# Kernel optimization log

Hardware: AMD Instinct MI355X
Metric: run time of the kernel (lower is better)

The kernel has to match this reference:

```python
import jax, jax.numpy as jnp
import numpy as np

B, S, D, H = 2, 2048, 1024, 16
DK = D // H


def setup_inputs() -> dict:
    key = jax.random.key(0)
    ks = jax.random.split(key, 12)
    scale = 1.0 / np.sqrt(D)
    inp = {
        "Q": jax.random.normal(ks[0], (B, S, D), jnp.float32),
        "K": jax.random.normal(ks[1], (B, S, D), jnp.float32),
        "V": jax.random.normal(ks[2], (B, S, D), jnp.float32),
        # causal mask, broadcast over batch: [B, S, S]
        "mask": jnp.broadcast_to(jnp.tril(jnp.ones((S, S), jnp.bool_)), (B, S, S)),
        "WQ_w": jax.random.normal(ks[3], (D, D), jnp.float32) * scale,
        "WQ_b": jnp.zeros((D,), jnp.float32),
        "WK_w": jax.random.normal(ks[4], (D, D), jnp.float32) * scale,
        "WK_b": jnp.zeros((D,), jnp.float32),
        "WV_w": jax.random.normal(ks[5], (D, D), jnp.float32) * scale,
        "WV_b": jnp.zeros((D,), jnp.float32),
        "WO_w": jax.random.normal(ks[6], (D, D), jnp.float32) * scale,
        "WO_b": jnp.zeros((D,), jnp.float32),
    }
    return inp


def reference(Q, K, V, mask, WQ_w, WQ_b, WK_w, WK_b, WV_w, WV_b, WO_w, WO_b):
    # Linear projections (torch Linear: x @ W.T + b), split heads -> [B,H,S,DK]
    def proj(x, w, b):
        return (x @ w.T + b).reshape(B, S, H, DK).transpose(0, 2, 1, 3)

    q = proj(Q, WQ_w, WQ_b)
    k = proj(K, WK_w, WK_b)
    v = proj(V, WV_w, WV_b)

    scores = jnp.einsum("bhqd,bhkd->bhqk", q, k) / jnp.sqrt(jnp.asarray(DK, q.dtype))
    scores = jnp.where(mask[:, None, :, :], scores, -jnp.inf)
    attn = jax.nn.softmax(scores, axis=-1)  # dropout is identity in eval mode

    out = jnp.einsum("bhqk,bhkd->bhqd", attn, v)
    out = out.transpose(0, 2, 1, 3).reshape(B, S, D)
    out = out @ WO_w.T + WO_b
    return (out, attn)
```

## Files before the change

kernel.cpp:

```cpp
#include <hip/hip_runtime.h>

#define S_LEN 2048
#define DMODEL 1024
#define NHEAD 16
#define DKH 64
#define BATCH 2

typedef __bf16 bf16_t;
typedef __bf16 bf16x8 __attribute__((ext_vector_type(8)));
typedef __bf16 bf16x4 __attribute__((ext_vector_type(4)));
typedef float f32x4 __attribute__((ext_vector_type(4)));

__device__ __forceinline__ void gload16(const bf16_t* g, bf16_t* l) {
  __builtin_amdgcn_global_load_lds(
      (const __attribute__((address_space(1))) unsigned int*)g,
      (__attribute__((address_space(3))) unsigned int*)l,
      16, 0, 0);
}

__global__ void cvt_all(const float* __restrict__ Q, const float* __restrict__ K,
                        const float* __restrict__ V, const float* __restrict__ WQ,
                        const float* __restrict__ WK, const float* __restrict__ WV,
                        const float* __restrict__ WO, bf16_t* __restrict__ dst) {
  const int i = blockIdx.x * 256 + threadIdx.x;
  const float* src;
  int off;
  if (i < 1572864) {
    const int seg = i >> 19;
    off = i & 524287;
    src = (seg == 0) ? Q : ((seg == 1) ? K : V);
  } else {
    const int j = i - 1572864;
    const int seg = j >> 17;
    off = j & 131071;
    src = (seg == 0) ? WQ : ((seg == 1) ? WK : ((seg == 2) ? WV : WO));
  }
  f32x4 a = *(const f32x4*)(src + (size_t)off * 8);
  f32x4 b = *(const f32x4*)(src + (size_t)off * 8 + 4);
  bf16x8 v;
#pragma unroll
  for (int j = 0; j < 4; ++j) { v[j] = (bf16_t)a[j]; v[4 + j] = (bf16_t)b[j]; }
  *(bf16x8*)(dst + (size_t)i * 8) = v;
}

struct GOp {
  const bf16_t* A;
  const bf16_t* W;
  const float* bias;
  char* out;
  int emode;
};

#define GM 4096
#define GN 1024
#define GK 1024
#define BM 128
#define BN 128
#define BK 64

__launch_bounds__(256, 2)
__global__ void gemm_bf16(GOp op0, GOp op1, GOp op2) {
  GOp op = (blockIdx.z == 0) ? op0 : ((blockIdx.z == 1) ? op1 : op2);
  const int n0 = blockIdx.x * BN;
  const int m0 = blockIdx.y * BM;
  const int t = threadIdx.x;
  const int w = t >> 6;
  const int l = t & 63;
  const int wr = w >> 1, wc = w & 1;
  const int lg = l >> 4, ll = l & 15;

  __shared__ __align__(16) bf16_t Asm[BM * BK];
  __shared__ __align__(16) bf16_t Bsm[BN * BK];

  f32x4 acc[4][4] = {};

  const int sr = l >> 3;
  const int sc = l & 7;

  for (int kt = 0; kt < GK / BK; ++kt) {
    __syncthreads();
#pragma unroll
    for (int i = 0; i < 4; ++i) {
      const int rbase = i * 32 + (w << 3);
      const int row = rbase + sr;
      const int gc = (sc ^ (row & 7)) << 3;
      gload16(op.A + (size_t)(m0 + row) * GK + kt * BK + gc, &Asm[rbase * BK]);
      gload16(op.W + (size_t)(n0 + row) * GK + kt * BK + gc, &Bsm[rbase * BK]);
    }
    __syncthreads();

    bf16x8 af[4][2], bfr[4][2];
#pragma unroll
    for (int mi = 0; mi < 4; ++mi) {
      const int row = wr * 64 + mi * 16 + ll;
      af[mi][0] = *(const bf16x8*)&Asm[row * BK + ((lg ^ (row & 7)) << 3)];
      af[mi][1] = *(const bf16x8*)&Asm[row * BK + (((4 + lg) ^ (row & 7)) << 3)];
    }
#pragma unroll
    for (int ni = 0; ni < 4; ++ni) {
      const int row = wc * 64 + ni * 16 + ll;
      bfr[ni][0] = *(const bf16x8*)&Bsm[row * BK + ((lg ^ (row & 7)) << 3)];
      bfr[ni][1] = *(const bf16x8*)&Bsm[row * BK + (((4 + lg) ^ (row & 7)) << 3)];
    }
#pragma unroll
    for (int mi = 0; mi < 4; ++mi)
#pragma unroll
      for (int ni = 0; ni < 4; ++ni) {
        acc[mi][ni] = __builtin_amdgcn_mfma_f32_16x16x32_bf16(af[mi][0], bfr[ni][0], acc[mi][ni], 0, 0, 0);
        acc[mi][ni] = __builtin_amdgcn_mfma_f32_16x16x32_bf16(af[mi][1], bfr[ni][1], acc[mi][ni], 0, 0, 0);
      }
  }

#pragma unroll
  for (int mi = 0; mi < 4; ++mi) {
#pragma unroll
    for (int ni = 0; ni < 4; ++ni) {
      const int col = n0 + wc * 64 + ni * 16 + ll;
      const int rbase = m0 + wr * 64 + mi * 16 + (lg << 2);
      const float bval = op.bias[col];
      f32x4 v = acc[mi][ni];
      if (op.emode == 0) {
        bf16_t* o = (bf16_t*)op.out;
#pragma unroll
        for (int r = 0; r < 4; ++r)
          o[(size_t)(rbase + r) * GN + col] = (bf16_t)(v[r] + bval);
      } else if (op.emode == 1) {
        const int hh = col >> 6, dd = col & 63;
        const int bb = rbase >> 11, ss = rbase & (S_LEN - 1);
        bf16_t* o = (bf16_t*)op.out + (((size_t)bb * NHEAD + hh) * DKH + dd) * S_LEN + ss;
        bf16x4 pk;
#pragma unroll
        for (int r = 0; r < 4; ++r) pk[r] = (bf16_t)(v[r] + bval);
        *(bf16x4*)o = pk;
      } else {
        float* o = (float*)op.out;
#pragma unroll
        for (int r = 0; r < 4; ++r)
          o[(size_t)(rbase + r) * GN + col] = v[r] + bval;
      }
    }
  }
}

__launch_bounds__(256, 2)
__global__ void attn2(const bf16_t* __restrict__ qp, const bf16_t* __restrict__ kp,
                      const bf16_t* __restrict__ vT, float* __restrict__ attn_out,
                      bf16_t* __restrict__ ctx) {
  const int raw = blockIdx.x;
  const int wg = (raw & 7) * 64 + (raw >> 3);
  const int bh = wg >> 4;
  const int pr = wg & 15;
  const int b = bh >> 4, h = bh & 15;
  const int flip = wg & 1;

  __shared__ __align__(16) bf16_t Qs[64 * 64];
  __shared__ __align__(16) bf16_t Ks[64 * 64];
  __shared__ __align__(16) bf16_t Vs[64 * 64];
  __shared__ __align__(16) bf16_t Pt[4][16 * 64];

  const int t = threadIdx.x;
  const int w = t >> 6;
  const int l = t & 63;
  const int lg = l >> 4;
  const int ll = l & 15;
  const int sr = l >> 3;
  const int sc = l & 7;

  for (int half = 0; half < 2; ++half) {
    const int qt = (half ^ flip) ? (31 - pr) : pr;
    const int q0 = qt * 64;
    const int nkt = qt + 1;

    __syncthreads();
#pragma unroll
    for (int i = 0; i < 2; ++i) {
      const int rbase = i * 32 + (w << 3);
      const int row = rbase + sr;
      const int gc = (sc ^ (row & 7)) << 3;
      gload16(qp + (size_t)(b * S_LEN + q0 + row) * DMODEL + h * DKH + gc, &Qs[rbase * 64]);
    }
    __syncthreads();

    bf16x8 qf0, qf1;
    {
      const int row = w * 16 + ll;
      qf0 = *(const bf16x8*)&Qs[row * 64 + ((lg ^ (row & 7)) << 3)];
      qf1 = *(const bf16x8*)&Qs[row * 64 + (((4 + lg) ^ (row & 7)) << 3)];
    }

    f32x4 oacc[4] = {};
    float sums[4] = {0.f, 0.f, 0.f, 0.f};
    const int qrow_base = q0 + w * 16 + (lg << 2);

    for (int kt = 0; kt < nkt; ++kt) {
      __syncthreads();
#pragma unroll
      for (int i = 0; i < 2; ++i) {
        const int rbase = i * 32 + (w << 3);
        const int row = rbase + sr;
        const int gc = (sc ^ (row & 7)) << 3;
        gload16(kp + (size_t)(b * S_LEN + kt * 64 + row) * DMODEL + h * DKH + gc, &Ks[rbase * 64]);
        gload16(vT + ((size_t)bh * DKH + row) * S_LEN + kt * 64 + gc, &Vs[rbase * 64]);
      }
      __syncthreads();

      const bool diag = (kt == qt);
#pragma unroll
      for (int cb = 0; cb < 4; ++cb) {
        const int krow = cb * 16 + ll;
        bf16x8 kf0 = *(const bf16x8*)&Ks[krow * 64 + ((lg ^ (krow & 7)) << 3)];
        bf16x8 kf1 = *(const bf16x8*)&Ks[krow * 64 + (((4 + lg) ^ (krow & 7)) << 3)];
        f32x4 a = {0.f, 0.f, 0.f, 0.f};
        a = __builtin_amdgcn_mfma_f32_16x16x32_bf16(qf0, kf0, a, 0, 0, 0);
        a = __builtin_amdgcn_mfma_f32_16x16x32_bf16(qf1, kf1, a, 0, 0, 0);
        const int gcol = kt * 64 + krow;
        if (diag) {
#pragma unroll
          for (int r = 0; r < 4; ++r) {
            const float e = (gcol <= qrow_base + r) ? __expf(a[r] * 0.125f) : 0.0f;
            sums[r] += e;
            const int ql = (lg << 2) + r;
            const int k = cb * 16 + ll;
            *(bf16_t*)((char*)&Pt[w][0] + ql * 128 + (((k >> 3) ^ (ql & 7)) << 4) + ((k & 7) << 1)) = (bf16_t)e;
          }
        } else {
#pragma unroll
          for (int r = 0; r < 4; ++r) {
            const float e = __expf(a[r] * 0.125f);
            sums[r] += e;
            const int ql = (lg << 2) + r;
            const int k = cb * 16 + ll;
            *(bf16_t*)((char*)&Pt[w][0] + ql * 128 + (((k >> 3) ^ (ql & 7)) << 4) + ((k & 7) << 1)) = (bf16_t)e;
          }
        }
      }
      bf16x8 pa0 = *(const bf16x8*)((char*)&Pt[w][0] + ll * 128 + ((lg ^ (ll & 7)) << 4));
      bf16x8 pa1 = *(const bf16x8*)((char*)&Pt[w][0] + ll * 128 + (((4 + lg) ^ (ll & 7)) << 4));
#pragma unroll
      for (int db = 0; db < 4; ++db) {
        const int drow = db * 16 + ll;
        bf16x8 vf0 = *(const bf16x8*)&Vs[drow * 64 + ((lg ^ (drow & 7)) << 3)];
        bf16x8 vf1 = *(const bf16x8*)&Vs[drow * 64 + (((4 + lg) ^ (drow & 7)) << 3)];
        oacc[db] = __builtin_amdgcn_mfma_f32_16x16x32_bf16(pa0, vf0, oacc[db], 0, 0, 0);
        oacc[db] = __builtin_amdgcn_mfma_f32_16x16x32_bf16(pa1, vf1, oacc[db], 0, 0, 0);
      }
    }

    float rinv[4];
#pragma unroll
    for (int r = 0; r < 4; ++r) {
      float s = sums[r];
      s += __shfl_xor(s, 1);
      s += __shfl_xor(s, 2);
      s += __shfl_xor(s, 4);
      s += __shfl_xor(s, 8);
      rinv[r] = 1.0f / s;
    }

#pragma unroll
    for (int db = 0; db < 4; ++db)
#pragma unroll
      for (int r = 0; r < 4; ++r) {
        const int grow = q0 + w * 16 + (lg << 2) + r;
        ctx[(size_t)(b * S_LEN + grow) * DMODEL + h * DKH + db * 16 + ll] = (bf16_t)(oacc[db][r] * rinv[r]);
      }

    float* arow = attn_out + ((size_t)bh * S_LEN + q0) * S_LEN;
    for (int kt = 0; kt <= qt; ++kt) {
      __syncthreads();
#pragma unroll
      for (int i = 0; i < 2; ++i) {
        const int rbase = i * 32 + (w << 3);
        const int row = rbase + sr;
        const int gc = (sc ^ (row & 7)) << 3;
        gload16(kp + (size_t)(b * S_LEN + kt * 64 + row) * DMODEL + h * DKH + gc, &Ks[rbase * 64]);
      }
      __syncthreads();

      const bool diag = (kt == qt);
#pragma unroll
      for (int cb = 0; cb < 4; ++cb) {
        const int krow = cb * 16 + ll;
        bf16x8 kf0 = *(const bf16x8*)&Ks[krow * 64 + ((lg ^ (krow & 7)) << 3)];
        bf16x8 kf1 = *(const bf16x8*)&Ks[krow * 64 + (((4 + lg) ^ (krow & 7)) << 3)];
        f32x4 a = {0.f, 0.f, 0.f, 0.f};
        a = __builtin_amdgcn_mfma_f32_16x16x32_bf16(qf0, kf0, a, 0, 0, 0);
        a = __builtin_amdgcn_mfma_f32_16x16x32_bf16(qf1, kf1, a, 0, 0, 0);
        const int gcol = kt * 64 + krow;
        if (diag) {
#pragma unroll
          for (int r = 0; r < 4; ++r) {
            const float e = (gcol <= qrow_base + r) ? __expf(a[r] * 0.125f) * rinv[r] : 0.0f;
            arow[(size_t)(w * 16 + (lg << 2) + r) * S_LEN + gcol] = e;
          }
        } else {
#pragma unroll
          for (int r = 0; r < 4; ++r)
            arow[(size_t)(w * 16 + (lg << 2) + r) * S_LEN + gcol] = __expf(a[r] * 0.125f) * rinv[r];
        }
      }
    }
    for (int kt = qt + 1; kt < 32; ++kt) {
      f32x4 z = {0.f, 0.f, 0.f, 0.f};
#pragma unroll
      for (int j = 0; j < 4; ++j) {
        const int row = w * 16 + (lg << 2) + j;
        *(f32x4*)(arow + (size_t)row * S_LEN + kt * 64 + (ll << 2)) = z;
      }
    }
  }
}

extern "C" void kernel_launch(void* const* d_in, const int* in_sizes, int n_in,
                              void* d_out, int out_size, void* d_ws, size_t ws_size,
                              hipStream_t stream) {
  const float* Q   = (const float*)d_in[0];
  const float* K   = (const float*)d_in[1];
  const float* V   = (const float*)d_in[2];
  const float* WQw = (const float*)d_in[4];
  const float* WQb = (const float*)d_in[5];
  const float* WKw = (const float*)d_in[6];
  const float* WKb = (const float*)d_in[7];
  const float* WVw = (const float*)d_in[8];
  const float* WVb = (const float*)d_in[9];
  const float* WOw = (const float*)d_in[10];
  const float* WOb = (const float*)d_in[11];

  char* ws = (char*)d_ws;
  bf16_t* qb  = (bf16_t*)(ws);
  bf16_t* kb  = (bf16_t*)(ws + (size_t)( 8 << 20));
  bf16_t* vb  = (bf16_t*)(ws + (size_t)(16 << 20));
  bf16_t* wq  = (bf16_t*)(ws + (size_t)(24 << 20));
  bf16_t* wk  = (bf16_t*)(ws + (size_t)(26 << 20));
  bf16_t* wv  = (bf16_t*)(ws + (size_t)(28 << 20));
  bf16_t* wo  = (bf16_t*)(ws + (size_t)(30 << 20));
  bf16_t* qp  = (bf16_t*)(ws + (size_t)(32 << 20));
  bf16_t* kp  = (bf16_t*)(ws + (size_t)(40 << 20));
  bf16_t* vT  = (bf16_t*)(ws + (size_t)(48 << 20));
  bf16_t* ctx = (bf16_t*)(ws + (size_t)(56 << 20));

  float* out_main = (float*)d_out;
  float* attn_out = out_main + (size_t)BATCH * S_LEN * DMODEL;

  cvt_all<<<dim3(8192), 256, 0, stream>>>(Q, K, V, WQw, WKw, WVw, WOw, (bf16_t*)ws);

  GOp opq{qb, wq, WQb, (char*)qp, 0};
  GOp opk{kb, wk, WKb, (char*)kp, 0};
  GOp opv{vb, wv, WVb, (char*)vT, 1};
  gemm_bf16<<<dim3(8, 32, 3), 256, 0, stream>>>(opq, opk, opv);

  attn2<<<dim3(512), 256, 0, stream>>>(qp, kp, vT, attn_out, ctx);

  GOp opo{ctx, wo, WOb, (char*)out_main, 2};
  gemm_bf16<<<dim3(8, 32, 1), 256, 0, stream>>>(opo, opo, opo);
}
```

Before: 224.5 us.

## Double-buffer LDS tiles in GEMM and attention kernels to overlap loads

Both the projection GEMM and the attention kernel now use two LDS buffers per operand. The next K/V (or A/W) tile is prefetched with global_load_lds while the current tile feeds the MFMAs, which replaces the load-then-sync pattern at the top of each iteration with a single barrier at the end. The aim is to hide global-memory latency behind matrix compute. The cost is doubled LDS use: 64KB per GEMM block, which could limit occupancy. The attention kernel is probably still bound by the large fp32 attention-matrix writes.

```diff
diff --git a/kernel.cpp b/kernel.cpp
--- a/kernel.cpp
+++ b/kernel.cpp
@@ -57,6 +57,7 @@
 #define BM 128
 #define BN 128
 #define BK 64
+#define NKT_G (GK / BK)
 
 __launch_bounds__(256, 2)
 __global__ void gemm_bf16(GOp op0, GOp op1, GOp op2) {
@@ -68,39 +69,46 @@
   const int l = t & 63;
   const int wr = w >> 1, wc = w & 1;
   const int lg = l >> 4, ll = l & 15;
-
-  __shared__ __align__(16) bf16_t Asm[BM * BK];
-  __shared__ __align__(16) bf16_t Bsm[BN * BK];
-
-  f32x4 acc[4][4] = {};
-
   const int sr = l >> 3;
   const int sc = l & 7;
 
-  for (int kt = 0; kt < GK / BK; ++kt) {
-    __syncthreads();
-#pragma unroll
-    for (int i = 0; i < 4; ++i) {
-      const int rbase = i * 32 + (w << 3);
-      const int row = rbase + sr;
-      const int gc = (sc ^ (row & 7)) << 3;
-      gload16(op.A + (size_t)(m0 + row) * GK + kt * BK + gc, &Asm[rbase * BK]);
-      gload16(op.W + (size_t)(n0 + row) * GK + kt * BK + gc, &Bsm[rbase * BK]);
-    }
-    __syncthreads();
+  __shared__ __align__(16) bf16_t Asm[2][BM * BK];
+  __shared__ __align__(16) bf16_t Bsm[2][BM * BK];
+
+  f32x4 acc[4][4] = {};
+
+  const bf16_t* Abase = op.A + (size_t)m0 * GK;
+  const bf16_t* Wbase = op.W + (size_t)n0 * GK;
+
+#define G_STAGE(bu, kt)                                                          \
+  {                                                                              \
+    _Pragma("unroll") for (int i = 0; i < 4; ++i) {                              \
+      const int rbase = i * 32 + (w << 3);                                       \
+      const int row = rbase + sr;                                                \
+      const int gc = (sc ^ (row & 7)) << 3;                                      \
+      gload16(Abase + (size_t)row * GK + (kt) * BK + gc, &Asm[bu][rbase * BK]);  \
+      gload16(Wbase + (size_t)row * GK + (kt) * BK + gc, &Bsm[bu][rbase * BK]);  \
+    }                                                                            \
+  }
+
+  G_STAGE(0, 0);
+  __syncthreads();
+  int cur = 0;
+  for (int kt = 0; kt < NKT_G; ++kt) {
+    if (kt + 1 < NKT_G) G_STAGE(cur ^ 1, kt + 1);
 
     bf16x8 af[4][2], bfr[4][2];
 #pragma unroll
     for (int mi = 0; mi < 4; ++mi) {
       const int row = wr * 64 + mi * 16 + ll;
-      af[mi][0] = *(const bf16x8*)&Asm[row * BK + ((lg ^ (row & 7)) << 3)];
-      af[mi][1] = *(const bf16x8*)&Asm[row * BK + (((4 + lg) ^ (row & 7)) << 3)];
+      af[mi][0] = *(const bf16x8*)&Asm[cur][row * BK + ((lg ^ (row & 7)) << 3)];
+      af[mi][1] = *(const bf16x8*)&Asm[cur][row * BK + (((4 + lg) ^ (row & 7)) << 3)];
     }
 #pragma unroll
     for (int ni = 0; ni < 4; ++ni) {
       const int row = wc * 64 + ni * 16 + ll;
-      bfr[ni][0] = *(const bf16x8*)&Bsm[row * BK + ((lg ^ (row & 7)) << 3)];
-      bfr[ni][1] = *(const bf16x8*)&Bsm[row * BK + (((4 + lg) ^ (row & 7)) << 3)];
+      bfr[ni][0] = *(const bf16x8*)&Bsm[cur][row * BK + ((lg ^ (row & 7)) << 3)];
+      bfr[ni][1] = *(const bf16x8*)&Bsm[cur][row * BK + (((4 + lg) ^ (row & 7)) << 3)];
     }
 #pragma unroll
     for (int mi = 0; mi < 4; ++mi)
@@ -109,6 +117,8 @@
         acc[mi][ni] = __builtin_amdgcn_mfma_f32_16x16x32_bf16(af[mi][0], bfr[ni][0], acc[mi][ni], 0, 0, 0);
         acc[mi][ni] = __builtin_amdgcn_mfma_f32_16x16x32_bf16(af[mi][1], bfr[ni][1], acc[mi][ni], 0, 0, 0);
       }
+    __syncthreads();
+    cur ^= 1;
   }
 
 #pragma unroll
@@ -154,8 +164,8 @@
   const int flip = wg & 1;
 
   __shared__ __align__(16) bf16_t Qs[64 * 64];
-  __shared__ __align__(16) bf16_t Ks[64 * 64];
-  __shared__ __align__(16) bf16_t Vs[64 * 64];
+  __shared__ __align__(16) bf16_t Ks[2][64 * 64];
+  __shared__ __align__(16) bf16_t Vs[2][64 * 64];
   __shared__ __align__(16) bf16_t Pt[4][16 * 64];
 
   const int t = threadIdx.x;
@@ -166,6 +176,30 @@
   const int sr = l >> 3;
   const int sc = l & 7;
 
+  const bf16_t* kbh = kp + (size_t)b * S_LEN * DMODEL + h * DKH;
+  const bf16_t* vbh = vT + (size_t)bh * DKH * S_LEN;
+
+#define KV_STAGE(bu, kt)                                                        \
+  {                                                                             \
+    _Pragma("unroll") for (int i = 0; i < 2; ++i) {                             \
+      const int rbase = i * 32 + (w << 3);                                      \
+      const int row = rbase + sr;                                               \
+      const int gc = (sc ^ (row & 7)) << 3;                                     \
+      gload16(kbh + (size_t)((kt) * 64 + row) * DMODEL + gc, &Ks[bu][rbase * 64]); \
+      gload16(vbh + (size_t)row * S_LEN + (kt) * 64 + gc, &Vs[bu][rbase * 64]); \
+    }                                                                           \
+  }
+
+#define K_STAGE(bu, kt)                                                         \
+  {                                                                             \
+    _Pragma("unroll") for (int i = 0; i < 2; ++i) {                             \
+      const int rbase = i * 32 + (w << 3);                                      \
+      const int row = rbase + sr;                                               \
+      const int gc = (sc ^ (row & 7)) << 3;                                     \
+      gload16(kbh + (size_t)((kt) * 64 + row) * DMODEL + gc, &Ks[bu][rbase * 64]); \
+    }                                                                           \
+  }
+
   for (int half = 0; half < 2; ++half) {
     const int qt = (half ^ flip) ? (31 - pr) : pr;
     const int q0 = qt * 64;
@@ -179,6 +213,7 @@
       const int gc = (sc ^ (row & 7)) << 3;
       gload16(qp + (size_t)(b * S_LEN + q0 + row) * DMODEL + h * DKH + gc, &Qs[rbase * 64]);
     }
+    KV_STAGE(0, 0);
     __syncthreads();
 
     bf16x8 qf0, qf1;
@@ -192,24 +227,16 @@
     float sums[4] = {0.f, 0.f, 0.f, 0.f};
     const int qrow_base = q0 + w * 16 + (lg << 2);
 
+    int cur = 0;
     for (int kt = 0; kt < nkt; ++kt) {
-      __syncthreads();
-#pragma unroll
-      for (int i = 0; i < 2; ++i) {
-        const int rbase = i * 32 + (w << 3);
-        const int row = rbase + sr;
-        const int gc = (sc ^ (row & 7)) << 3;
-        gload16(kp + (size_t)(b * S_LEN + kt * 64 + row) * DMODEL + h * DKH + gc, &Ks[rbase * 64]);
-        gload16(vT + ((size_t)bh * DKH + row) * S_LEN + kt * 64 + gc, &Vs[rbase * 64]);
-      }
-      __syncthreads();
+      if (kt + 1 < nkt) KV_STAGE(cur ^ 1, kt + 1);
 
       const bool diag = (kt == qt);
 #pragma unroll
       for (int cb = 0; cb < 4; ++cb) {
         const int krow = cb * 16 + ll;
-        bf16x8 kf0 = *(const bf16x8*)&Ks[krow * 64 + ((lg ^ (krow & 7)) << 3)];
-        bf16x8 kf1 = *(const bf16x8*)&Ks[krow * 64 + (((4 + lg) ^ (krow & 7)) << 3)];
+        bf16x8 kf0 = *(const bf16x8*)&Ks[cur][krow * 64 + ((lg ^ (krow & 7)) << 3)];
+        bf16x8 kf1 = *(const bf16x8*)&Ks[cur][krow * 64 + (((4 + lg) ^ (krow & 7)) << 3)];
         f32x4 a = {0.f, 0.f, 0.f, 0.f};
         a = __builtin_amdgcn_mfma_f32_16x16x32_bf16(qf0, kf0, a, 0, 0, 0);
         a = __builtin_amdgcn_mfma_f32_16x16x32_bf16(qf1, kf1, a, 0, 0, 0);
@@ -239,12 +266,16 @@
 #pragma unroll
       for (int db = 0; db < 4; ++db) {
         const int drow = db * 16 + ll;
-        bf16x8 vf0 = *(const bf16x8*)&Vs[drow * 64 + ((lg ^ (drow & 7)) << 3)];
-        bf16x8 vf1 = *(const bf16x8*)&Vs[drow * 64 + (((4 + lg) ^ (drow & 7)) << 3)];
+        bf16x8 vf0 = *(const bf16x8*)&Vs[cur][drow * 64 + ((lg ^ (drow & 7)) << 3)];
+        bf16x8 vf1 = *(const bf16x8*)&Vs[cur][drow * 64 + (((4 + lg) ^ (drow & 7)) << 3)];
         oacc[db] = __builtin_amdgcn_mfma_f32_16x16x32_bf16(pa0, vf0, oacc[db], 0, 0, 0);
         oacc[db] = __builtin_amdgcn_mfma_f32_16x16x32_bf16(pa1, vf1, oacc[db], 0, 0, 0);
       }
-    }
+      __syncthreads();
+      cur ^= 1;
+    }
+
+    K_STAGE(0, 0);
 
     float rinv[4];
 #pragma unroll
@@ -256,6 +287,7 @@
       s += __shfl_xor(s, 8);
       rinv[r] = 1.0f / s;
     }
+    __syncthreads();
 
 #pragma unroll
     for (int db = 0; db < 4; ++db)
@@ -266,23 +298,16 @@
       }
 
     float* arow = attn_out + ((size_t)bh * S_LEN + q0) * S_LEN;
+    int cur2 = 0;
     for (int kt = 0; kt <= qt; ++kt) {
-      __syncthreads();
-#pragma unroll
-      for (int i = 0; i < 2; ++i) {
-        const int rbase = i * 32 + (w << 3);
-        const int row = rbase + sr;
-        const int gc = (sc ^ (row & 7)) << 3;
-        gload16(kp + (size_t)(b * S_LEN + kt * 64 + row) * DMODEL + h * DKH + gc, &Ks[rbase * 64]);
-      }
-      __syncthreads();
+      if (kt + 1 <= qt) K_STAGE(cur2 ^ 1, kt + 1);
 
       const bool diag = (kt == qt);
 #pragma unroll
       for (int cb = 0; cb < 4; ++cb) {
         const int krow = cb * 16 + ll;
-        bf16x8 kf0 = *(const bf16x8*)&Ks[krow * 64 + ((lg ^ (krow & 7)) << 3)];
-        bf16x8 kf1 = *(const bf16x8*)&Ks[krow * 64 + (((4 + lg) ^ (krow & 7)) << 3)];
+        bf16x8 kf0 = *(const bf16x8*)&Ks[cur2][krow * 64 + ((lg ^ (krow & 7)) << 3)];
+        bf16x8 kf1 = *(const bf16x8*)&Ks[cur2][krow * 64 + (((4 + lg) ^ (krow & 7)) << 3)];
         f32x4 a = {0.f, 0.f, 0.f, 0.f};
         a = __builtin_amdgcn_mfma_f32_16x16x32_bf16(qf0, kf0, a, 0, 0, 0);
         a = __builtin_amdgcn_mfma_f32_16x16x32_bf16(qf1, kf1, a, 0, 0, 0);
@@ -299,6 +324,8 @@
             arow[(size_t)(w * 16 + (lg << 2) + r) * S_LEN + gcol] = __expf(a[r] * 0.125f) * rinv[r];
         }
       }
+      __syncthreads();
+      cur2 ^= 1;
     }
     for (int kt = qt + 1; kt < 32; ++kt) {
       f32x4 z = {0.f, 0.f, 0.f, 0.f};
```

Result: no change. 226.8 us (+1.0%).

## Split attention into ctx pass and fused prob-write plus output-projection tail kernel

Applied to the files above, without the earlier changes.

The single attention kernel is split in two. The first computes the context with double-buffered K/V tiles and saves the per-row inverse softmax sums to workspace. A second kernel runs the attention-probability write pass alongside the output projection GEMM as extra blocks in the same launch, so the memory-bound prob writes can overlap with compute-bound GEMM work. Occupancy is raised to four blocks per CU, and the P scratch reuses the Q shared buffer. The costs are an extra round trip for rinv and a 64x64-tile output GEMM with less data reuse.

```diff
diff --git a/kernel.cpp b/kernel.cpp
--- a/kernel.cpp
+++ b/kernel.cpp
@@ -68,14 +68,13 @@
   const int l = t & 63;
   const int wr = w >> 1, wc = w & 1;
   const int lg = l >> 4, ll = l & 15;
-
-  __shared__ __align__(16) bf16_t Asm[BM * BK];
-  __shared__ __align__(16) bf16_t Bsm[BN * BK];
-
-  f32x4 acc[4][4] = {};
-
   const int sr = l >> 3;
   const int sc = l & 7;
+
+  __shared__ __align__(16) bf16_t Asm[BM * BK];
+  __shared__ __align__(16) bf16_t Bsm[BM * BK];
+
+  f32x4 acc[4][4] = {};
 
   for (int kt = 0; kt < GK / BK; ++kt) {
     __syncthreads();
@@ -124,7 +123,7 @@
 #pragma unroll
         for (int r = 0; r < 4; ++r)
           o[(size_t)(rbase + r) * GN + col] = (bf16_t)(v[r] + bval);
-      } else if (op.emode == 1) {
+      } else {
         const int hh = col >> 6, dd = col & 63;
         const int bb = rbase >> 11, ss = rbase & (S_LEN - 1);
         bf16_t* o = (bf16_t*)op.out + (((size_t)bb * NHEAD + hh) * DKH + dd) * S_LEN + ss;
@@ -132,52 +131,174 @@
 #pragma unroll
         for (int r = 0; r < 4; ++r) pk[r] = (bf16_t)(v[r] + bval);
         *(bf16x4*)o = pk;
-      } else {
-        float* o = (float*)op.out;
-#pragma unroll
-        for (int r = 0; r < 4; ++r)
-          o[(size_t)(rbase + r) * GN + col] = v[r] + bval;
-      }
-    }
-  }
-}
-
-__launch_bounds__(256, 2)
-__global__ void attn2(const bf16_t* __restrict__ qp, const bf16_t* __restrict__ kp,
-                      const bf16_t* __restrict__ vT, float* __restrict__ attn_out,
-                      bf16_t* __restrict__ ctx) {
+      }
+    }
+  }
+}
+
+__launch_bounds__(256, 4)
+__global__ void attn_ctx(const bf16_t* __restrict__ qp, const bf16_t* __restrict__ kp,
+                         const bf16_t* __restrict__ vT, bf16_t* __restrict__ ctx,
+                         float* __restrict__ rinv_ws) {
   const int raw = blockIdx.x;
-  const int wg = (raw & 7) * 64 + (raw >> 3);
-  const int bh = wg >> 4;
-  const int pr = wg & 15;
+  const int wg = (raw & 7) * 128 + (raw >> 3);
+  const int bh = wg >> 5;
+  const int i5 = wg & 31;
+  const int qt = (i5 & 1) ? (31 - (i5 >> 1)) : (i5 >> 1);
   const int b = bh >> 4, h = bh & 15;
-  const int flip = wg & 1;
+  const int q0 = qt * 64;
+  const int nkt = qt + 1;
 
   __shared__ __align__(16) bf16_t Qs[64 * 64];
-  __shared__ __align__(16) bf16_t Ks[64 * 64];
-  __shared__ __align__(16) bf16_t Vs[64 * 64];
-  __shared__ __align__(16) bf16_t Pt[4][16 * 64];
+  __shared__ __align__(16) bf16_t Ks[2][64 * 64];
+  __shared__ __align__(16) bf16_t Vs[2][64 * 64];
 
   const int t = threadIdx.x;
   const int w = t >> 6;
   const int l = t & 63;
-  const int lg = l >> 4;
-  const int ll = l & 15;
-  const int sr = l >> 3;
-  const int sc = l & 7;
-
-  for (int half = 0; half < 2; ++half) {
-    const int qt = (half ^ flip) ? (31 - pr) : pr;
+  const int lg = l >> 4, ll = l & 15;
+  const int sr = l >> 3, sc = l & 7;
+
+  const bf16_t* kbh = kp + (size_t)b * S_LEN * DMODEL + h * DKH;
+  const bf16_t* vbh = vT + (size_t)bh * DKH * S_LEN;
+  char* PtW = (char*)Qs + (w << 11);
+
+#pragma unroll
+  for (int i = 0; i < 2; ++i) {
+    const int rbase = i * 32 + (w << 3);
+    const int row = rbase + sr;
+    const int gc = (sc ^ (row & 7)) << 3;
+    gload16(qp + (size_t)(b * S_LEN + q0 + row) * DMODEL + h * DKH + gc, &Qs[rbase * 64]);
+    gload16(kbh + (size_t)row * DMODEL + gc, &Ks[0][rbase * 64]);
+    gload16(vbh + (size_t)row * S_LEN + gc, &Vs[0][rbase * 64]);
+  }
+  __syncthreads();
+
+  bf16x8 qf0, qf1;
+  {
+    const int row = w * 16 + ll;
+    qf0 = *(const bf16x8*)&Qs[row * 64 + ((lg ^ (row & 7)) << 3)];
+    qf1 = *(const bf16x8*)&Qs[row * 64 + (((4 + lg) ^ (row & 7)) << 3)];
+  }
+
+  f32x4 oacc[4] = {};
+  float sums[4] = {0.f, 0.f, 0.f, 0.f};
+  const int qrow_base = q0 + w * 16 + (lg << 2);
+
+  int cur = 0;
+  for (int kt = 0; kt < nkt; ++kt) {
+    if (kt + 1 < nkt) {
+#pragma unroll
+      for (int i = 0; i < 2; ++i) {
+        const int rbase = i * 32 + (w << 3);
+        const int row = rbase + sr;
+        const int gc = (sc ^ (row & 7)) << 3;
+        gload16(kbh + (size_t)((kt + 1) * 64 + row) * DMODEL + gc, &Ks[cur ^ 1][rbase * 64]);
+        gload16(vbh + (size_t)row * S_LEN + (kt + 1) * 64 + gc, &Vs[cur ^ 1][rbase * 64]);
+      }
+    }
+    const bool diag = (kt == qt);
+#pragma unroll
+    for (int cb = 0; cb < 4; ++cb) {
+      const int krow = cb * 16 + ll;
+      bf16x8 kf0 = *(const bf16x8*)&Ks[cur][krow * 64 + ((lg ^ (krow & 7)) << 3)];
+      bf16x8 kf1 = *(const bf16x8*)&Ks[cur][krow * 64 + (((4 + lg) ^ (krow & 7)) << 3)];
+      f32x4 a = {0.f, 0.f, 0.f, 0.f};
+      a = __builtin_amdgcn_mfma_f32_16x16x32_bf16(qf0, kf0, a, 0, 0, 0);
+      a = __builtin_amdgcn_mfma_f32_16x16x32_bf16(qf1, kf1, a, 0, 0, 0);
+      const int gcol = kt * 64 + krow;
+      if (diag) {
+#pragma unroll
+        for (int r = 0; r < 4; ++r) {
+          const float e = (gcol <= qrow_base + r) ? __expf(a[r] * 0.125f) : 0.0f;
+          sums[r] += e;
+          const int ql = (lg << 2) + r;
+          const int k = cb * 16 + ll;
+          *(bf16_t*)(PtW + ql * 128 + (((k >> 3) ^ (ql & 7)) << 4) + ((k & 7) << 1)) = (bf16_t)e;
+        }
+      } else {
+#pragma unroll
+        for (int r = 0; r < 4; ++r) {
+          const float e = __expf(a[r] * 0.125f);
+          sums[r] += e;
+          const int ql = (lg << 2) + r;
+          const int k = cb * 16 + ll;
+          *(bf16_t*)(PtW + ql * 128 + (((k >> 3) ^ (ql & 7)) << 4) + ((k & 7) << 1)) = (bf16_t)e;
+        }
+      }
+    }
+    bf16x8 pa0 = *(const bf16x8*)(PtW + ll * 128 + ((lg ^ (ll & 7)) << 4));
+    bf16x8 pa1 = *(const bf16x8*)(PtW + ll * 128 + (((4 + lg) ^ (ll & 7)) << 4));
+#pragma unroll
+    for (int db = 0; db < 4; ++db) {
+      const int drow = db * 16 + ll;
+      bf16x8 vf0 = *(const bf16x8*)&Vs[cur][drow * 64 + ((lg ^ (drow & 7)) << 3)];
+      bf16x8 vf1 = *(const bf16x8*)&Vs[cur][drow * 64 + (((4 + lg) ^ (drow & 7)) << 3)];
+      oacc[db] = __builtin_amdgcn_mfma_f32_16x16x32_bf16(pa0, vf0, oacc[db], 0, 0, 0);
+      oacc[db] = __builtin_amdgcn_mfma_f32_16x16x32_bf16(pa1, vf1, oacc[db], 0, 0, 0);
+    }
+    __syncthreads();
+    cur ^= 1;
+  }
+
+  float rinv[4];
+#pragma unroll
+  for (int r = 0; r < 4; ++r) {
+    float s = sums[r];
+    s += __shfl_xor(s, 1);
+    s += __shfl_xor(s, 2);
+    s += __shfl_xor(s, 4);
+    s += __shfl_xor(s, 8);
+    rinv[r] = 1.0f / s;
+  }
+  if (ll == 0) {
+#pragma unroll
+    for (int r = 0; r < 4; ++r) rinv_ws[(size_t)bh * S_LEN + qrow_base + r] = rinv[r];
+  }
+
+#pragma unroll
+  for (int db = 0; db < 4; ++db)
+#pragma unroll
+    for (int r = 0; r < 4; ++r) {
+      const int grow = q0 + w * 16 + (lg << 2) + r;
+      ctx[(size_t)(b * S_LEN + grow) * DMODEL + h * DKH + db * 16 + ll] = (bf16_t)(oacc[db][r] * rinv[r]);
+    }
+}
+
+__launch_bounds__(256, 4)
+__global__ void fused_tail(const bf16_t* __restrict__ qp, const bf16_t* __restrict__ kp,
+                           const float* __restrict__ rinv_ws, float* __restrict__ attn_out,
+                           const bf16_t* __restrict__ ctxA, const bf16_t* __restrict__ woW,
+                           const float* __restrict__ wob, float* __restrict__ out_main) {
+  __shared__ __align__(16) char smem[24576];
+  const int t = threadIdx.x;
+  const int w = t >> 6;
+  const int l = t & 63;
+  const int lg = l >> 4, ll = l & 15;
+  const int sr = l >> 3, sc = l & 7;
+
+  if (blockIdx.x < 1024) {
+    const int raw = blockIdx.x;
+    const int wg = (raw & 7) * 128 + (raw >> 3);
+    const int bh = wg >> 5;
+    const int i5 = wg & 31;
+    const int qt = (i5 & 1) ? (31 - (i5 >> 1)) : (i5 >> 1);
+    const int b = bh >> 4, h = bh & 15;
     const int q0 = qt * 64;
-    const int nkt = qt + 1;
-
-    __syncthreads();
+
+    bf16_t* Qs = (bf16_t*)smem;
+    bf16_t* Ks0 = (bf16_t*)(smem + 8192);
+    bf16_t* Ks1 = (bf16_t*)(smem + 16384);
+
+    const bf16_t* kbh = kp + (size_t)b * S_LEN * DMODEL + h * DKH;
+
 #pragma unroll
     for (int i = 0; i < 2; ++i) {
       const int rbase = i * 32 + (w << 3);
       const int row = rbase + sr;
       const int gc = (sc ^ (row & 7)) << 3;
       gload16(qp + (size_t)(b * S_LEN + q0 + row) * DMODEL + h * DKH + gc, &Qs[rbase * 64]);
+      gload16(kbh + (size_t)row * DMODEL + gc, &Ks0[rbase * 64]);
     }
     __syncthreads();
 
@@ -187,29 +308,31 @@
       qf0 = *(const bf16x8*)&Qs[row * 64 + ((lg ^ (row & 7)) << 3)];
       qf1 = *(const bf16x8*)&Qs[row * 64 + (((4 + lg) ^ (row & 7)) << 3)];
     }
-
-    f32x4 oacc[4] = {};
-    float sums[4] = {0.f, 0.f, 0.f, 0.f};
     const int qrow_base = q0 + w * 16 + (lg << 2);
-
-    for (int kt = 0; kt < nkt; ++kt) {
-      __syncthreads();
-#pragma unroll
-      for (int i = 0; i < 2; ++i) {
-        const int rbase = i * 32 + (w << 3);
-        const int row = rbase + sr;
-        const int gc = (sc ^ (row & 7)) << 3;
-        gload16(kp + (size_t)(b * S_LEN + kt * 64 + row) * DMODEL + h * DKH + gc, &Ks[rbase * 64]);
-        gload16(vT + ((size_t)bh * DKH + row) * S_LEN + kt * 64 + gc, &Vs[rbase * 64]);
-      }
-      __syncthreads();
-
+    float rinv[4];
+#pragma unroll
+    for (int r = 0; r < 4; ++r) rinv[r] = rinv_ws[(size_t)bh * S_LEN + qrow_base + r];
+
+    float* arow = attn_out + ((size_t)bh * S_LEN + q0) * S_LEN;
+    int cur = 0;
+    for (int kt = 0; kt <= qt; ++kt) {
+      bf16_t* Kc = cur ? Ks1 : Ks0;
+      bf16_t* Kn = cur ? Ks0 : Ks1;
+      if (kt + 1 <= qt) {
+#pragma unroll
+        for (int i = 0; i < 2; ++i) {
+          const int rbase = i * 32 + (w << 3);
+          const int row = rbase + sr;
+          const int gc = (sc ^ (row & 7)) << 3;
+          gload16(kbh + (size_t)((kt + 1) * 64 + row) * DMODEL + gc, &Kn[rbase * 64]);
+        }
+      }
       const bool diag = (kt == qt);
 #pragma unroll
       for (int cb = 0; cb < 4; ++cb) {
         const int krow = cb * 16 + ll;
-        bf16x8 kf0 = *(const bf16x8*)&Ks[krow * 64 + ((lg ^ (krow & 7)) << 3)];
-        bf16x8 kf1 = *(const bf16x8*)&Ks[krow * 64 + (((4 + lg) ^ (krow & 7)) << 3)];
+        bf16x8 kf0 = *(const bf16x8*)&Kc[krow * 64 + ((lg ^ (krow & 7)) << 3)];
+        bf16x8 kf1 = *(const bf16x8*)&Kc[krow * 64 + (((4 + lg) ^ (krow & 7)) << 3)];
         f32x4 a = {0.f, 0.f, 0.f, 0.f};
         a = __builtin_amdgcn_mfma_f32_16x16x32_bf16(qf0, kf0, a, 0, 0, 0);
         a = __builtin_amdgcn_mfma_f32_16x16x32_bf16(qf1, kf1, a, 0, 0, 0);
@@ -217,96 +340,69 @@
         if (diag) {
 #pragma unroll
           for (int r = 0; r < 4; ++r) {
-            const float e = (gcol <= qrow_base + r) ? __expf(a[r] * 0.125f) : 0.0f;
-            sums[r] += e;
-            const int ql = (lg << 2) + r;
-            const int k = cb * 16 + ll;
-            *(bf16_t*)((char*)&Pt[w][0] + ql * 128 + (((k >> 3) ^ (ql & 7)) << 4) + ((k & 7) << 1)) = (bf16_t)e;
+            const float e = (gcol <= qrow_base + r) ? __expf(a[r] * 0.125f) * rinv[r] : 0.0f;
+            arow[(size_t)(w * 16 + (lg << 2) + r) * S_LEN + gcol] = e;
           }
         } else {
 #pragma unroll
-          for (int r = 0; r < 4; ++r) {
-            const float e = __expf(a[r] * 0.125f);
-            sums[r] += e;
-            const int ql = (lg << 2) + r;
-            const int k = cb * 16 + ll;
-            *(bf16_t*)((char*)&Pt[w][0] + ql * 128 + (((k >> 3) ^ (ql & 7)) << 4) + ((k & 7) << 1)) = (bf16_t)e;
-          }
+          for (int r = 0; r < 4; ++r)
+            arow[(size_t)(w * 16 + (lg << 2) + r) * S_LEN + gcol] = __expf(a[r] * 0.125f) * rinv[r];
         }
       }
-      bf16x8 pa0 = *(const bf16x8*)((char*)&Pt[w][0] + ll * 128 + ((lg ^ (ll & 7)) << 4));
-      bf16x8 pa1 = *(const bf16x8*)((char*)&Pt[w][0] + ll * 128 + (((4 + lg) ^ (ll & 7)) << 4));
-#pragma unroll
-      for (int db = 0; db < 4; ++db) {
-        const int drow = db * 16 + ll;
-        bf16x8 vf0 = *(const bf16x8*)&Vs[drow * 64 + ((lg ^ (drow & 7)) << 3)];
-        bf16x8 vf1 = *(const bf16x8*)&Vs[drow * 64 + (((4 + lg) ^ (drow & 7)) << 3)];
-        oacc[db] = __builtin_amdgcn_mfma_f32_16x16x32_bf16(pa0, vf0, oacc[db], 0, 0, 0);
-        oacc[db] = __builtin_amdgcn_mfma_f32_16x16x32_bf16(pa1, vf1, oacc[db], 0, 0, 0);
-      }
-    }
-
-    float rinv[4];
-#pragma unroll
-    for (int r = 0; r < 4; ++r) {
-      float s = sums[r];
-      s += __shfl_xor(s, 1);
-      s += __shfl_xor(s, 2);
-      s += __shfl_xor(s, 4);
-      s += __shfl_xor(s, 8);
-      rinv[r] = 1.0f / s;
-    }
-
-#pragma unroll
-    for (int db = 0; db < 4; ++db)
-#pragma unroll
-      for (int r = 0; r < 4; ++r) {
-        const int grow = q0 + w * 16 + (lg << 2) + r;
-        ctx[(size_t)(b * S_LEN + grow) * DMODEL + h * DKH + db * 16 + ll] = (bf16_t)(oacc[db][r] * rinv[r]);
-      }
-
-    float* arow = attn_out + ((size_t)bh * S_LEN + q0) * S_LEN;
-    for (int kt = 0; kt <= qt; ++kt) {
+      __syncthreads();
+      cur ^= 1;
+    }
+    for (int kt = qt + 1; kt < 32; ++kt) {
+      f32x4 z = {0.f, 0.f, 0.f, 0.f};
+#pragma unroll
+      for (int j = 0; j < 4; ++j) {
+        const int row = w * 16 + (lg << 2) + j;
+        *(f32x4*)(arow + (size_t)row * S_LEN + kt * 64 + (ll << 2)) = z;
+      }
+    }
+  } else {
+    const int bid = blockIdx.x - 1024;
+    const int m0 = (bid >> 4) * 64;
+    const int n0 = (bid & 15) * 64;
+    bf16_t* As = (bf16_t*)smem;
+    bf16_t* Bs = (bf16_t*)(smem + 8192);
+
+    f32x4 acc[4] = {};
+    const bf16_t* Ab = ctxA + (size_t)m0 * GK;
+    const bf16_t* Wb = woW + (size_t)n0 * GK;
+
+    for (int kt = 0; kt < GK / 64; ++kt) {
       __syncthreads();
 #pragma unroll
       for (int i = 0; i < 2; ++i) {
         const int rbase = i * 32 + (w << 3);
         const int row = rbase + sr;
         const int gc = (sc ^ (row & 7)) << 3;
-        gload16(kp + (size_t)(b * S_LEN + kt * 64 + row) * DMODEL + h * DKH + gc, &Ks[rbase * 64]);
+        gload16(Ab + (size_t)row * GK + kt * 64 + gc, &As[rbase * 64]);
+        gload16(Wb + (size_t)row * GK + kt * 64 + gc, &Bs[rbase * 64]);
       }
       __syncthreads();
 
-      const bool diag = (kt == qt);
+      const int arw = w * 16 + ll;
+      bf16x8 af0 = *(const bf16x8*)&As[arw * 64 + ((lg ^ (arw & 7)) << 3)];
+      bf16x8 af1 = *(const bf16x8*)&As[arw * 64 + (((4 + lg) ^ (arw & 7)) << 3)];
 #pragma unroll
       for (int cb = 0; cb < 4; ++cb) {
-        const int krow = cb * 16 + ll;
-        bf16x8 kf0 = *(const bf16x8*)&Ks[krow * 64 + ((lg ^ (krow & 7)) << 3)];
-        bf16x8 kf1 = *(const bf16x8*)&Ks[krow * 64 + (((4 + lg) ^ (krow & 7)) << 3)];
-        f32x4 a = {0.f, 0.f, 0.f, 0.f};
-        a = __builtin_amdgcn_mfma_f32_16x16x32_bf16(qf0, kf0, a, 0, 0, 0);
-        a = __builtin_amdgcn_mfma_f32_16x16x32_bf16(qf1, kf1, a, 0, 0, 0);
-        const int gcol = kt * 64 + krow;
-        if (diag) {
-#pragma unroll
-          for (int r = 0; r < 4; ++r) {
-            const float e = (gcol <= qrow_base + r) ? __expf(a[r] * 0.125f) * rinv[r] : 0.0f;
-            arow[(size_t)(w * 16 + (lg << 2) + r) * S_LEN + gcol] = e;
-          }
-        } else {
-#pragma unroll
-          for (int r = 0; r < 4; ++r)
-            arow[(size_t)(w * 16 + (lg << 2) + r) * S_LEN + gcol] = __expf(a[r] * 0.125f) * rinv[r];
-        }
-      }
-    }
-    for (int kt = qt + 1; kt < 32; ++kt) {
-      f32x4 z = {0.f, 0.f, 0.f, 0.f};
-#pragma unroll
-      for (int j = 0; j < 4; ++j) {
-        const int row = w * 16 + (lg << 2) + j;
-        *(f32x4*)(arow + (size_t)row * S_LEN + kt * 64 + (ll << 2)) = z;
-      }
+        const int brow = cb * 16 + ll;
+        bf16x8 bf0 = *(const bf16x8*)&Bs[brow * 64 + ((lg ^ (brow & 7)) << 3)];
+        bf16x8 bf1 = *(const bf16x8*)&Bs[brow * 64 + (((4 + lg) ^ (brow & 7)) << 3)];
+        acc[cb] = __builtin_amdgcn_mfma_f32_16x16x32_bf16(af0, bf0, acc[cb], 0, 0, 0);
+        acc[cb] = __builtin_amdgcn_mfma_f32_16x16x32_bf16(af1, bf1, acc[cb], 0, 0, 0);
+      }
+    }
+#pragma unroll
+    for (int cb = 0; cb < 4; ++cb) {
+      const int col = n0 + cb * 16 + ll;
+      const float bval = wob[col];
+      const int rb = m0 + w * 16 + (lg << 2);
+#pragma unroll
+      for (int r = 0; r < 4; ++r)
+        out_main[(size_t)(rb + r) * GN + col] = acc[cb][r] + bval;
     }
   }
 }
@@ -338,6 +434,7 @@
   bf16_t* kp  = (bf16_t*)(ws + (size_t)(40 << 20));
   bf16_t* vT  = (bf16_t*)(ws + (size_t)(48 << 20));
   bf16_t* ctx = (bf16_t*)(ws + (size_t)(56 << 20));
+  float* rinv_ws = (float*)ws;
 
   float* out_main = (float*)d_out;
   float* attn_out = out_main + (size_t)BATCH * S_LEN * DMODEL;
@@ -349,8 +446,7 @@
   GOp opv{vb, wv, WVb, (char*)vT, 1};
   gemm_bf16<<<dim3(8, 32, 3), 256, 0, stream>>>(opq, opk, opv);
 
-  attn2<<<dim3(512), 256, 0, stream>>>(qp, kp, vT, attn_out, ctx);
-
-  GOp opo{ctx, wo, WOb, (char*)out_main, 2};
-  gemm_bf16<<<dim3(8, 32, 1), 256, 0, stream>>>(opo, opo, opo);
-}
+  attn_ctx<<<dim3(1024), 256, 0, stream>>>(qp, kp, vT, ctx, rinv_ws);
+
+  fused_tail<<<dim3(2048), 256, 0, stream>>>(qp, kp, rinv_ws, attn_out, ctx, wo, WOb, out_main);
+}
```

New measurement: 267.6 us. +19.2%, slower.

## Double-buffer K/V tiles in attention and vectorize attn-prob stores via transposed MFMA

Applied to the files above, without the earlier changes.

The attention kernel now double-buffers K and V tiles in shared memory, prefetching the next tile while the current one is computed, and drops one barrier per iteration. The probability-writing pass computes K·Qᵀ instead of Q·Kᵀ, so each lane holds four consecutive key columns and writes them as one 16-byte store. The per-row reciprocal sums are passed through shared memory for this. Launch bounds are raised to 3 waves per SIMD on both kernels, which may force register spills, and the extra buffers add LDS use that could limit occupancy.

```diff
diff --git a/kernel.cpp b/kernel.cpp
--- a/kernel.cpp
+++ b/kernel.cpp
@@ -58,7 +58,7 @@
 #define BN 128
 #define BK 64
 
-__launch_bounds__(256, 2)
+__launch_bounds__(256, 3)
 __global__ void gemm_bf16(GOp op0, GOp op1, GOp op2) {
   GOp op = (blockIdx.z == 0) ? op0 : ((blockIdx.z == 1) ? op1 : op2);
   const int n0 = blockIdx.x * BN;
@@ -68,14 +68,13 @@
   const int l = t & 63;
   const int wr = w >> 1, wc = w & 1;
   const int lg = l >> 4, ll = l & 15;
-
-  __shared__ __align__(16) bf16_t Asm[BM * BK];
-  __shared__ __align__(16) bf16_t Bsm[BN * BK];
-
-  f32x4 acc[4][4] = {};
-
   const int sr = l >> 3;
   const int sc = l & 7;
+
+  __shared__ __align__(16) bf16_t Asm[BM * BK];
+  __shared__ __align__(16) bf16_t Bsm[BM * BK];
+
+  f32x4 acc[4][4] = {};
 
   for (int kt = 0; kt < GK / BK; ++kt) {
     __syncthreads();
@@ -142,7 +141,7 @@
   }
 }
 
-__launch_bounds__(256, 2)
+__launch_bounds__(256, 3)
 __global__ void attn2(const bf16_t* __restrict__ qp, const bf16_t* __restrict__ kp,
                       const bf16_t* __restrict__ vT, float* __restrict__ attn_out,
                       bf16_t* __restrict__ ctx) {
@@ -154,9 +153,10 @@
   const int flip = wg & 1;
 
   __shared__ __align__(16) bf16_t Qs[64 * 64];
-  __shared__ __align__(16) bf16_t Ks[64 * 64];
-  __shared__ __align__(16) bf16_t Vs[64 * 64];
+  __shared__ __align__(16) bf16_t Ks[2][64 * 64];
+  __shared__ __align__(16) bf16_t Vs[2][64 * 64];
   __shared__ __align__(16) bf16_t Pt[4][16 * 64];
+  __shared__ float rinvS[64];
 
   const int t = threadIdx.x;
   const int w = t >> 6;
@@ -166,6 +166,30 @@
   const int sr = l >> 3;
   const int sc = l & 7;
 
+  const bf16_t* kbh = kp + (size_t)b * S_LEN * DMODEL + h * DKH;
+  const bf16_t* vbh = vT + (size_t)bh * DKH * S_LEN;
+
+#define KV_STAGE(bu, kt)                                                           \
+  {                                                                                \
+    _Pragma("unroll") for (int i = 0; i < 2; ++i) {                                \
+      const int rbase = i * 32 + (w << 3);                                         \
+      const int row = rbase + sr;                                                  \
+      const int gc = (sc ^ (row & 7)) << 3;                                        \
+      gload16(kbh + (size_t)((kt) * 64 + row) * DMODEL + gc, &Ks[bu][rbase * 64]); \
+      gload16(vbh + (size_t)row * S_LEN + (kt) * 64 + gc, &Vs[bu][rbase * 64]);    \
+    }                                                                              \
+  }
+
+#define K_STAGE(bu, kt)                                                            \
+  {                                                                                \
+    _Pragma("unroll") for (int i = 0; i < 2; ++i) {                                \
+      const int rbase = i * 32 + (w << 3);                                         \
+      const int row = rbase + sr;                                                  \
+      const int gc = (sc ^ (row & 7)) << 3;                                        \
+      gload16(kbh + (size_t)((kt) * 64 + row) * DMODEL + gc, &Ks[bu][rbase * 64]); \
+    }                                                                              \
+  }
+
   for (int half = 0; half < 2; ++half) {
     const int qt = (half ^ flip) ? (31 - pr) : pr;
     const int q0 = qt * 64;
@@ -179,6 +203,7 @@
       const int gc = (sc ^ (row & 7)) << 3;
       gload16(qp + (size_t)(b * S_LEN + q0 + row) * DMODEL + h * DKH + gc, &Qs[rbase * 64]);
     }
+    KV_STAGE(0, 0);
     __syncthreads();
 
     bf16x8 qf0, qf1;
@@ -192,24 +217,16 @@
     float sums[4] = {0.f, 0.f, 0.f, 0.f};
     const int qrow_base = q0 + w * 16 + (lg << 2);
 
+    int cur = 0;
     for (int kt = 0; kt < nkt; ++kt) {
-      __syncthreads();
-#pragma unroll
-      for (int i = 0; i < 2; ++i) {
-        const int rbase = i * 32 + (w << 3);
-        const int row = rbase + sr;
-        const int gc = (sc ^ (row & 7)) << 3;
-        gload16(kp + (size_t)(b * S_LEN + kt * 64 + row) * DMODEL + h * DKH + gc, &Ks[rbase * 64]);
-        gload16(vT + ((size_t)bh * DKH + row) * S_LEN + kt * 64 + gc, &Vs[rbase * 64]);
-      }
-      __syncthreads();
+      if (kt + 1 < nkt) KV_STAGE(cur ^ 1, kt + 1);
 
       const bool diag = (kt == qt);
 #pragma unroll
       for (int cb = 0; cb < 4; ++cb) {
         const int krow = cb * 16 + ll;
-        bf16x8 kf0 = *(const bf16x8*)&Ks[krow * 64 + ((lg ^ (krow & 7)) << 3)];
-        bf16x8 kf1 = *(const bf16x8*)&Ks[krow * 64 + (((4 + lg) ^ (krow & 7)) << 3)];
+        bf16x8 kf0 = *(const bf16x8*)&Ks[cur][krow * 64 + ((lg ^ (krow & 7)) << 3)];
+        bf16x8 kf1 = *(const bf16x8*)&Ks[cur][krow * 64 + (((4 + lg) ^ (krow & 7)) << 3)];
         f32x4 a = {0.f, 0.f, 0.f, 0.f};
         a = __builtin_amdgcn_mfma_f32_16x16x32_bf16(qf0, kf0, a, 0, 0, 0);
         a = __builtin_amdgcn_mfma_f32_16x16x32_bf16(qf1, kf1, a, 0, 0, 0);
@@ -239,11 +256,13 @@
 #pragma unroll
       for (int db = 0; db < 4; ++db) {
         const int drow = db * 16 + ll;
-        bf16x8 vf0 = *(const bf16x8*)&Vs[drow * 64 + ((lg ^ (drow & 7)) << 3)];
-        bf16x8 vf1 = *(const bf16x8*)&Vs[drow * 64 + (((4 + lg) ^ (drow & 7)) << 3)];
+        bf16x8 vf0 = *(const bf16x8*)&Vs[cur][drow * 64 + ((lg ^ (drow & 7)) << 3)];
+        bf16x8 vf1 = *(const bf16x8*)&Vs[cur][drow * 64 + (((4 + lg) ^ (drow & 7)) << 3)];
         oacc[db] = __builtin_amdgcn_mfma_f32_16x16x32_bf16(pa0, vf0, oacc[db], 0, 0, 0);
         oacc[db] = __builtin_amdgcn_mfma_f32_16x16x32_bf16(pa1, vf1, oacc[db], 0, 0, 0);
       }
+      __syncthreads();
+      cur ^= 1;
     }
 
     float rinv[4];
@@ -256,6 +275,12 @@
       s += __shfl_xor(s, 8);
       rinv[r] = 1.0f / s;
     }
+    if (ll == 0) {
+#pragma unroll
+      for (int r = 0; r < 4; ++r) rinvS[w * 16 + (lg << 2) + r] = rinv[r];
+    }
+
+    K_STAGE(0, 0);
 
 #pragma unroll
     for (int db = 0; db < 4; ++db)
@@ -264,42 +289,11 @@
         const int grow = q0 + w * 16 + (lg << 2) + r;
         ctx[(size_t)(b * S_LEN + grow) * DMODEL + h * DKH + db * 16 + ll] = (bf16_t)(oacc[db][r] * rinv[r]);
       }
-
+    __syncthreads();
+
+    const float rv = rinvS[w * 16 + ll];
     float* arow = attn_out + ((size_t)bh * S_LEN + q0) * S_LEN;
-    for (int kt = 0; kt <= qt; ++kt) {
-      __syncthreads();
-#pragma unroll
-      for (int i = 0; i < 2; ++i) {
-        const int rbase = i * 32 + (w << 3);
-        const int row = rbase + sr;
-        const int gc = (sc ^ (row & 7)) << 3;
-        gload16(kp + (size_t)(b * S_LEN + kt * 64 + row) * DMODEL + h * DKH + gc, &Ks[rbase * 64]);
-      }
-      __syncthreads();
-
-      const bool diag = (kt == qt);
-#pragma unroll
-      for (int cb = 0; cb < 4; ++cb) {
-        const int krow = cb * 16 + ll;
-        bf16x8 kf0 = *(const bf16x8*)&Ks[krow * 64 + ((lg ^ (krow & 7)) << 3)];
-        bf16x8 kf1 = *(const bf16x8*)&Ks[krow * 64 + (((4 + lg) ^ (krow & 7)) << 3)];
-        f32x4 a = {0.f, 0.f, 0.f, 0.f};
-        a = __builtin_amdgcn_mfma_f32_16x16x32_bf16(qf0, kf0, a, 0, 0, 0);
-        a = __builtin_amdgcn_mfma_f32_16x16x32_bf16(qf1, kf1, a, 0, 0, 0);
-        const int gcol = kt * 64 + krow;
-        if (diag) {
-#pragma unroll
-          for (int r = 0; r < 4; ++r) {
-            const float e = (gcol <= qrow_base + r) ? __expf(a[r] * 0.125f) * rinv[r] : 0.0f;
-            arow[(size_t)(w * 16 + (lg << 2) + r) * S_LEN + gcol] = e;
-          }
-        } else {
-#pragma unroll
-          for (int r = 0; r < 4; ++r)
-            arow[(size_t)(w * 16 + (lg << 2) + r) * S_LEN + gcol] = __expf(a[r] * 0.125f) * rinv[r];
-        }
-      }
-    }
+
     for (int kt = qt + 1; kt < 32; ++kt) {
       f32x4 z = {0.f, 0.f, 0.f, 0.f};
 #pragma unroll
@@ -308,7 +302,39 @@
         *(f32x4*)(arow + (size_t)row * S_LEN + kt * 64 + (ll << 2)) = z;
       }
     }
-  }
+
+    const int qrow_sw = q0 + w * 16 + ll;
+    int cur2 = 0;
+    for (int kt = 0; kt <= qt; ++kt) {
+      if (kt + 1 <= qt) K_STAGE(cur2 ^ 1, kt + 1);
+
+      const bool diag = (kt == qt);
+#pragma unroll
+      for (int i = 0; i < 4; ++i) {
+        const int krow = i * 16 + ll;
+        bf16x8 kf0 = *(const bf16x8*)&Ks[cur2][krow * 64 + ((lg ^ (krow & 7)) << 3)];
+        bf16x8 kf1 = *(const bf16x8*)&Ks[cur2][krow * 64 + (((4 + lg) ^ (krow & 7)) << 3)];
+        f32x4 a = {0.f, 0.f, 0.f, 0.f};
+        a = __builtin_amdgcn_mfma_f32_16x16x32_bf16(kf0, qf0, a, 0, 0, 0);
+        a = __builtin_amdgcn_mfma_f32_16x16x32_bf16(kf1, qf1, a, 0, 0, 0);
+        const int kbase = kt * 64 + i * 16 + (lg << 2);
+        f32x4 o;
+        if (diag) {
+#pragma unroll
+          for (int r = 0; r < 4; ++r)
+            o[r] = (kbase + r <= qrow_sw) ? __expf(a[r] * 0.125f) * rv : 0.0f;
+        } else {
+#pragma unroll
+          for (int r = 0; r < 4; ++r) o[r] = __expf(a[r] * 0.125f) * rv;
+        }
+        *(f32x4*)(arow + (size_t)(w * 16 + ll) * S_LEN + kbase) = o;
+      }
+      __syncthreads();
+      cur2 ^= 1;
+    }
+  }
+#undef KV_STAGE
+#undef K_STAGE
 }
 
 extern "C" void kernel_launch(void* const* d_in, const int* in_sizes, int n_in,
```

After: 229.4 us. 1.02x slower.
